# Kernel optimization log

Hardware: AMD Instinct MI355X
Metric: run time of the kernel (lower is better)

## Reference

```python
import jax, jax.numpy as jnp
import numpy as np

B, S, D, H, M = 2, 2048, 1024, 16, 4096
DH = D // H
EPS = 1e-6  # flax LayerNorm default
THETA = 10000.0


def layer_norm(x, scale, bias):
    m = jnp.mean(x, axis=-1, keepdims=True)
    v = jnp.var(x, axis=-1, keepdims=True)
    return (x - m) * jax.lax.rsqrt(v + EPS) * scale + bias


def apply_rope(xq, xk):
    # xq, xk: [B, S, H, DH]; rotate consecutive pairs as complex numbers
    half = DH // 2
    freqs = 1.0 / THETA ** (jnp.arange(0, DH, 2)[:half].astype(jnp.float32) / DH)
    t = jnp.arange(S, dtype=jnp.float32)
    ang = jnp.outer(t, freqs)                      # [S, half]
    cos = jnp.cos(ang)[None, :, None, :]           # [1, S, 1, half]
    sin = jnp.sin(ang)[None, :, None, :]

    def rot(x):
        xr = x.astype(jnp.float32).reshape(*x.shape[:-1], half, 2)
        a, b = xr[..., 0], xr[..., 1]
        out = jnp.stack((a * cos - b * sin, a * sin + b * cos), axis=-1)
        return out.reshape(*x.shape).astype(jnp.float32)

    return rot(xq), rot(xk)


def setup_inputs() -> dict:
    key = jax.random.key(0)
    ks = jax.random.split(key, 12)
    sd = 1.0 / np.sqrt(D)
    return {
        "x": jax.random.normal(ks[0], (B, S, D), jnp.float32),
        "ln1_s": jnp.ones((D,), jnp.float32),
        "ln1_b": jnp.zeros((D,), jnp.float32),
        "wk": jax.random.normal(ks[1], (D, D), jnp.float32) * sd,
        "wq": jax.random.normal(ks[2], (D, D), jnp.float32) * sd,
        "wv": jax.random.normal(ks[3], (D, D), jnp.float32) * sd,
        "wo": jax.random.normal(ks[4], (D, D), jnp.float32) * sd,
        "ln2_s": jnp.ones((D,), jnp.float32),
        "ln2_b": jnp.zeros((D,), jnp.float32),
        "w1": jax.random.normal(ks[5], (D, M), jnp.float32) * sd,
        "b1": jnp.zeros((M,), jnp.float32),
        "w2": jax.random.normal(ks[6], (M, D), jnp.float32) * (1.0 / np.sqrt(M)),
        "b2": jnp.zeros((D,), jnp.float32),
    }


def reference(x, ln1_s, ln1_b, wk, wq, wv, wo, ln2_s, ln2_b, w1, b1, w2, b2):
    h = layer_norm(x, ln1_s, ln1_b)
    xk = (h @ wk).reshape(B, S, H, DH)
    xq = (h @ wq).reshape(B, S, H, DH)
    xv = (h @ wv).reshape(B, S, H, DH)
    xq, xk = apply_rope(xq, xk)
    # scores: [B, H, S, S]
    scores = jnp.einsum("bqhd,bkhd->bhqk", xq, xk) / jnp.sqrt(jnp.float32(DH))
    attn = jax.nn.softmax(scores, axis=-1)
    ctx = jnp.einsum("bhqk,bkhd->bqhd", attn, xv).reshape(B, S, D)
    attn_out = ctx @ wo
    mlp_in = attn_out + x
    h2 = layer_norm(mlp_in, ln2_s, ln2_b)
    h2 = jax.nn.gelu(h2 @ w1 + b1)  # approximate gelu (jax default, matches source)
    h2 = h2 @ w2 + b2
    return h2 + mlp_in
```

## Files before the change

kernel.cpp:

```cpp
#include <hip/hip_runtime.h>
#include <stdint.h>

#define B_ 2
#define S_ 2048
#define D_ 1024
#define H_ 16
#define DH_ 64
#define M_ 4096
#define BS_ 4096

typedef __attribute__((ext_vector_type(8))) short short8;
typedef __attribute__((ext_vector_type(4))) float f32x4;

static __device__ __forceinline__ unsigned short f2bf(float f) {
  unsigned u = __float_as_uint(f);
  u += 0x7fffu + ((u >> 16) & 1u);
  return (unsigned short)(u >> 16);
}
static __device__ __forceinline__ float bf2f(unsigned short s) {
  return __uint_as_float(((unsigned)s) << 16);
}
static __device__ __forceinline__ f32x4 MFMA16(short8 a, short8 b, f32x4 c) {
  return __builtin_amdgcn_mfma_f32_16x16x32_bf16(a, b, c, 0, 0, 0);
}
static __device__ __forceinline__ void gload_lds16(const void* g, void* l) {
  __builtin_amdgcn_global_load_lds(
      (const __attribute__((address_space(1))) unsigned int*)g,
      (__attribute__((address_space(3))) unsigned int*)l, 16, 0, 0);
}
static __device__ __forceinline__ unsigned cvtpk_bf16(float lo, float hi) {
  unsigned r;
  asm("v_cvt_pk_bf16_f32 %0, %1, %2" : "=v"(r) : "v"(lo), "v"(hi));
  return r;
}
static __device__ __forceinline__ float gelu_f(float x) {
  float u = 0.7978845608028654f * (x + 0.044715f * x * x * x);
  return 0.5f * x * (1.0f + tanhf(u));
}

__global__ __launch_bounds__(256) void tcast_kernel(const float* __restrict__ in,
                                                    unsigned short* __restrict__ out,
                                                    int R, int C) {
  __shared__ float tile[32][33];
  int tx = threadIdx.x & 31, ty = threadIdx.x >> 5;
  int r0 = blockIdx.y * 32, c0 = blockIdx.x * 32;
#pragma unroll
  for (int i = 0; i < 4; ++i)
    tile[ty + i * 8][tx] = in[(size_t)(r0 + ty + i * 8) * C + c0 + tx];
  __syncthreads();
#pragma unroll
  for (int i = 0; i < 4; ++i)
    out[(size_t)(c0 + ty + i * 8) * R + r0 + tx] = f2bf(tile[tx][ty + i * 8]);
}

__global__ __launch_bounds__(256) void ln_kernel(const float* __restrict__ x,
                                                 const float* __restrict__ sc,
                                                 const float* __restrict__ bi,
                                                 unsigned short* __restrict__ out) {
  int row = blockIdx.x;
  int t = threadIdx.x;
  float4 v = ((const float4*)(x + (size_t)row * D_))[t];
  float s1 = v.x + v.y + v.z + v.w;
  float s2 = v.x * v.x + v.y * v.y + v.z * v.z + v.w * v.w;
#pragma unroll
  for (int m = 1; m < 64; m <<= 1) {
    s1 += __shfl_xor(s1, m);
    s2 += __shfl_xor(s2, m);
  }
  __shared__ float red[8];
  int w = t >> 6, l = t & 63;
  if (l == 0) { red[w] = s1; red[4 + w] = s2; }
  __syncthreads();
  s1 = red[0] + red[1] + red[2] + red[3];
  s2 = red[4] + red[5] + red[6] + red[7];
  float mean = s1 * (1.0f / D_);
  float var = s2 * (1.0f / D_) - mean * mean;
  float rstd = rsqrtf(var + 1e-6f);
  float4 scv = ((const float4*)sc)[t];
  float4 biv = ((const float4*)bi)[t];
  ushort4 o;
  o.x = f2bf((v.x - mean) * rstd * scv.x + biv.x);
  o.y = f2bf((v.y - mean) * rstd * scv.y + biv.y);
  o.z = f2bf((v.z - mean) * rstd * scv.z + biv.z);
  o.w = f2bf((v.w - mean) * rstd * scv.w + biv.w);
  ((ushort4*)out)[(size_t)row * (D_ / 4) + t] = o;
}

__global__ __launch_bounds__(256) void rope_kernel(unsigned short* __restrict__ t_,
                                                   float qscale) {
  size_t idx = (size_t)blockIdx.x * 256 + threadIdx.x;
  int c = (int)(idx & 7);
  size_t rowi = idx >> 3;
  int s = (int)(rowi & (S_ - 1));
  unsigned short* p = t_ + rowi * DH_ + c * 8;
  short8 v = *(const short8*)p;
  unsigned short o[8];
#pragma unroll
  for (int i = 0; i < 4; ++i) {
    int pi = c * 4 + i;
    float freq = exp2f(-(float)pi * 0.4152410118609203f);
    float ang = (float)s * freq;
    float sn, cs;
    sincosf(ang, &sn, &cs);
    float a = bf2f((unsigned short)v[2 * i]);
    float b = bf2f((unsigned short)v[2 * i + 1]);
    o[2 * i] = f2bf((a * cs - b * sn) * qscale);
    o[2 * i + 1] = f2bf((a * sn + b * cs) * qscale);
  }
  short8 ov;
#pragma unroll
  for (int i = 0; i < 8; ++i) ov[i] = (short)o[i];
  *(short8*)p = ov;
}

__global__ __launch_bounds__(256) void attn_kernel(const unsigned short* __restrict__ q,
                                                   const unsigned short* __restrict__ k,
                                                   const unsigned short* __restrict__ vt,
                                                   unsigned short* __restrict__ ctx) {
  __shared__ char smem[40960];
  const int tid = threadIdx.x, w = tid >> 6, l = tid & 63;
  const int g = l >> 4, qi = l & 15;
  char* Ps = smem + 32768 + w * 2048;
  int flat = blockIdx.y * 32 + blockIdx.x;
  int swz = (flat & 7) * 128 + (flat >> 3);
  const int bh = swz >> 5;
  const int b = bh >> 4, h = bh & 15;
  const int q0 = (swz & 31) * 64 + w * 16;

  const unsigned short* qbase = q + ((size_t)bh * S_ + q0 + qi) * DH_ + g * 8;
  short8 qf0 = *(const short8*)qbase;
  short8 qf1 = *(const short8*)(qbase + 32);

  const unsigned short* kb = k + (size_t)bh * S_ * DH_;
  const unsigned short* vb = vt + (size_t)bh * DH_ * S_;

  short8 onesB;
#pragma unroll
  for (int i = 0; i < 8; ++i) onesB[i] = (short)0x3F80;

  f32x4 o[4], l_acc;
#pragma unroll
  for (int dt = 0; dt < 4; ++dt) { f32x4 z = {0.f, 0.f, 0.f, 0.f}; o[dt] = z; }
  { f32x4 z = {0.f, 0.f, 0.f, 0.f}; l_acc = z; }

#define STAGE_KV(buf, kt)                                                        \
  {                                                                              \
    char* Ks_ = smem + (buf) * 16384;                                            \
    char* Vs_ = Ks_ + 8192;                                                      \
    _Pragma("unroll") for (int i = 0; i < 2; ++i) {                              \
      int slot = i * 256 + tid;                                                  \
      int r = slot >> 3, pc = slot & 7;                                          \
      int sc_ = pc ^ (r & 7);                                                    \
      gload_lds16(kb + (size_t)((kt) + r) * DH_ + sc_ * 8,                       \
                  Ks_ + (i * 4096 + w * 1024));                                  \
      gload_lds16(vb + (size_t)r * S_ + (kt) + sc_ * 8,                          \
                  Vs_ + (i * 4096 + w * 1024));                                  \
    }                                                                            \
  }

  STAGE_KV(0, 0);
  asm volatile("s_waitcnt vmcnt(0)" ::: "memory");
  __builtin_amdgcn_s_barrier();

  for (int t = 0; t < S_ / 64; ++t) {
    int buf = t & 1;
    if (t + 1 < S_ / 64) STAGE_KV(buf ^ 1, (t + 1) * 64);
    char* Ks = smem + buf * 16384;
    char* Vs = Ks + 8192;

#pragma unroll
    for (int jt = 0; jt < 4; ++jt) {
      int r = jt * 16 + qi;
      const char* krow = Ks + r * 128;
      short8 kf0 = *(const short8*)(krow + ((g ^ (r & 7)) << 4));
      short8 kf1 = *(const short8*)(krow + (((g + 4) ^ (r & 7)) << 4));
      f32x4 z = {0.f, 0.f, 0.f, 0.f};
      z = MFMA16(kf0, qf0, z);
      z = MFMA16(kf1, qf1, z);
      uint2 pk2;
      pk2.x = cvtpk_bf16(exp2f(z[0]), exp2f(z[1]));
      pk2.y = cvtpk_bf16(exp2f(z[2]), exp2f(z[3]));
      int slot = 2 * jt + (g >> 1);
      *(uint2*)(Ps + qi * 128 + ((slot ^ (qi & 7)) << 4) + (g & 1) * 8) = pk2;
    }

    short8 pa0 = *(const short8*)(Ps + qi * 128 + ((g ^ (qi & 7)) << 4));
    short8 pa1 = *(const short8*)(Ps + qi * 128 + (((g + 4) ^ (qi & 7)) << 4));
    l_acc = MFMA16(pa0, onesB, l_acc);
    l_acc = MFMA16(pa1, onesB, l_acc);
#pragma unroll
    for (int dt = 0; dt < 4; ++dt) {
      int r = dt * 16 + qi;
      const char* vrow = Vs + r * 128;
      short8 vf0 = *(const short8*)(vrow + ((g ^ (r & 7)) << 4));
      short8 vf1 = *(const short8*)(vrow + (((g + 4) ^ (r & 7)) << 4));
      o[dt] = MFMA16(pa0, vf0, o[dt]);
      o[dt] = MFMA16(pa1, vf1, o[dt]);
    }
    asm volatile("s_waitcnt vmcnt(0)" ::: "memory");
    __builtin_amdgcn_s_barrier();
  }

  float rl[4];
#pragma unroll
  for (int r = 0; r < 4; ++r) rl[r] = 1.0f / l_acc[r];
#pragma unroll
  for (int dt = 0; dt < 4; ++dt) {
#pragma unroll
    for (int r = 0; r < 4; ++r) {
      int s = q0 + 4 * g + r;
      ctx[((size_t)(b * S_) + s) * D_ + h * DH_ + dt * 16 + qi] =
          f2bf(o[dt][r] * rl[r]);
    }
  }
#undef STAGE_KV
}

template <int EPI>
__global__ __launch_bounds__(256) void gemm_bt(const unsigned short* __restrict__ A,
                                               const unsigned short* __restrict__ Bt,
                                               int K,
                                               const float* __restrict__ aux0,
                                               const float* __restrict__ aux1,
                                               void* __restrict__ out0,
                                               void* __restrict__ out1,
                                               void* __restrict__ out2) {
  __shared__ char smem[65536];
  int tid = threadIdx.x, w = tid >> 6, l = tid & 63;
  int wr = w >> 1, wc = w & 1;
  int gx = gridDim.x;
  int nwg = gx * gridDim.y;
  int flat = blockIdx.y * gx + blockIdx.x;
  int swz = (flat & 7) * (nwg >> 3) + (flat >> 3);
  int row0 = (swz / gx) * 128, col0 = (swz % gx) * 128;
  f32x4 acc[4][4];
#pragma unroll
  for (int mt = 0; mt < 4; ++mt)
#pragma unroll
    for (int nt = 0; nt < 4; ++nt) {
      f32x4 z = {0.f, 0.f, 0.f, 0.f};
      acc[mt][nt] = z;
    }
  int lr = l >> 3, lc = l & 7;

#define STAGE_AB(buf, kt)                                                        \
  {                                                                              \
    char* As_ = smem + (buf) * 32768;                                            \
    char* Bs_ = As_ + 16384;                                                     \
    _Pragma("unroll") for (int i = 0; i < 4; ++i) {                              \
      int rb = w * 32 + i * 8;                                                   \
      int r = rb + lr;                                                           \
      int sc_ = lc ^ (r & 7);                                                    \
      gload_lds16(A + (size_t)(row0 + r) * K + (kt) + sc_ * 8, As_ + rb * 128);  \
      gload_lds16(Bt + (size_t)(col0 + r) * K + (kt) + sc_ * 8, Bs_ + rb * 128); \
    }                                                                            \
  }

  STAGE_AB(0, 0);
  asm volatile("s_waitcnt vmcnt(0)" ::: "memory");
  __builtin_amdgcn_s_barrier();

  const int NT = K >> 6;
  for (int t = 0; t < NT; ++t) {
    int buf = t & 1;
    if (t + 1 < NT) STAGE_AB(buf ^ 1, (t + 1) * 64);
    char* As = smem + buf * 32768;
    char* Bs = As + 16384;
#pragma unroll
    for (int kf = 0; kf < 2; ++kf) {
      short8 af[4], bfr[4];
#pragma unroll
      for (int mt = 0; mt < 4; ++mt) {
        int r = wr * 64 + mt * 16 + (l & 15);
        int c = (l >> 4) + 4 * kf;
        af[mt] = *(const short8*)(As + r * 128 + ((c ^ (r & 7)) << 4));
      }
#pragma unroll
      for (int nt = 0; nt < 4; ++nt) {
        int r = wc * 64 + nt * 16 + (l & 15);
        int c = (l >> 4) + 4 * kf;
        bfr[nt] = *(const short8*)(Bs + r * 128 + ((c ^ (r & 7)) << 4));
      }
#pragma unroll
      for (int mt = 0; mt < 4; ++mt)
#pragma unroll
        for (int nt = 0; nt < 4; ++nt)
          acc[mt][nt] = MFMA16(af[mt], bfr[nt], acc[mt][nt]);
    }
    asm volatile("s_waitcnt vmcnt(0)" ::: "memory");
    __builtin_amdgcn_s_barrier();
  }
#undef STAGE_AB

#pragma unroll
  for (int mt = 0; mt < 4; ++mt) {
#pragma unroll
    for (int nt = 0; nt < 4; ++nt) {
      int grow0 = row0 + wr * 64 + mt * 16 + ((l >> 4) << 2);
      int gcol = col0 + wc * 64 + nt * 16 + (l & 15);
      if (EPI == 0) {
        int which = gcol >> 10;
        int d = gcol & 1023;
        int hh = d >> 6, dh = d & 63;
#pragma unroll
        for (int r = 0; r < 4; ++r) {
          int grow = grow0 + r;
          int b = grow >> 11, s = grow & 2047;
          float v = acc[mt][nt][r];
          if (which == 0)
            ((unsigned short*)out0)[(((size_t)(b * H_ + hh)) * S_ + s) * DH_ + dh] = f2bf(v);
          else if (which == 1)
            ((unsigned short*)out1)[(((size_t)(b * H_ + hh)) * S_ + s) * DH_ + dh] = f2bf(v);
          else
            ((unsigned short*)out2)[(((size_t)(b * H_ + hh)) * DH_ + dh) * S_ + s] = f2bf(v);
        }
      } else if (EPI == 1) {
        float* mo = (float*)out0;
#pragma unroll
        for (int r = 0; r < 4; ++r) {
          int grow = grow0 + r;
          mo[(size_t)grow * D_ + gcol] = acc[mt][nt][r] + aux0[(size_t)grow * D_ + gcol];
        }
      } else if (EPI == 2) {
        unsigned short* gq = (unsigned short*)out0;
        float bb = aux0[gcol];
#pragma unroll
        for (int r = 0; r < 4; ++r) {
          int grow = grow0 + r;
          gq[(size_t)grow * M_ + gcol] = f2bf(gelu_f(acc[mt][nt][r] + bb));
        }
      } else {
        float* po = (float*)out0;
        float bb = aux0[gcol];
#pragma unroll
        for (int r = 0; r < 4; ++r) {
          int grow = grow0 + r;
          po[(size_t)grow * D_ + gcol] =
              acc[mt][nt][r] + bb + aux1[(size_t)grow * D_ + gcol];
        }
      }
    }
  }
}

extern "C" void kernel_launch(void* const* d_in, const int* in_sizes, int n_in,
                              void* d_out, int out_size, void* d_ws, size_t ws_size,
                              hipStream_t stream) {
  const float* x = (const float*)d_in[0];
  const float* ln1s = (const float*)d_in[1];
  const float* ln1b = (const float*)d_in[2];
  const float* wk = (const float*)d_in[3];
  const float* wq = (const float*)d_in[4];
  const float* wv = (const float*)d_in[5];
  const float* wo = (const float*)d_in[6];
  const float* ln2s = (const float*)d_in[7];
  const float* ln2b = (const float*)d_in[8];
  const float* w1 = (const float*)d_in[9];
  const float* b1 = (const float*)d_in[10];
  const float* w2 = (const float*)d_in[11];
  const float* b2 = (const float*)d_in[12];

  char* ws = (char*)d_ws;
  unsigned short* wqkv_t = (unsigned short*)(ws);
  unsigned short* wo_t = (unsigned short*)(ws + 6291456);
  unsigned short* w1_t = (unsigned short*)(ws + 8388608);
  unsigned short* w2_t = (unsigned short*)(ws + 16777216);
  unsigned short* h_bf = (unsigned short*)(ws + 25165824);
  unsigned short* q_bf = (unsigned short*)(ws + 33554432);
  unsigned short* k_bf = (unsigned short*)(ws + 41943040);
  unsigned short* vt_bf = (unsigned short*)(ws + 50331648);
  unsigned short* ctx_bf = (unsigned short*)(ws + 58720256);
  float* mlp_in = (float*)(ws + 67108864);
  unsigned short* g_bf = (unsigned short*)(ws + 83886080);

  dim3 blk(256);
  tcast_kernel<<<dim3(32, 32), blk, 0, stream>>>(wq, wqkv_t, 1024, 1024);
  tcast_kernel<<<dim3(32, 32), blk, 0, stream>>>(wk, wqkv_t + 1048576, 1024, 1024);
  tcast_kernel<<<dim3(32, 32), blk, 0, stream>>>(wv, wqkv_t + 2097152, 1024, 1024);
  tcast_kernel<<<dim3(32, 32), blk, 0, stream>>>(wo, wo_t, 1024, 1024);
  tcast_kernel<<<dim3(128, 32), blk, 0, stream>>>(w1, w1_t, 1024, 4096);
  tcast_kernel<<<dim3(32, 128), blk, 0, stream>>>(w2, w2_t, 4096, 1024);
  ln_kernel<<<dim3(BS_), blk, 0, stream>>>(x, ln1s, ln1b, h_bf);
  gemm_bt<0><<<dim3(24, 32), blk, 0, stream>>>(h_bf, wqkv_t, 1024, nullptr, nullptr,
                                               q_bf, k_bf, vt_bf);
  rope_kernel<<<dim3(2048), blk, 0, stream>>>(q_bf, 0.125f * 1.4426950408889634f);
  rope_kernel<<<dim3(2048), blk, 0, stream>>>(k_bf, 1.0f);
  attn_kernel<<<dim3(32, 32), blk, 0, stream>>>(q_bf, k_bf, vt_bf, ctx_bf);
  gemm_bt<1><<<dim3(8, 32), blk, 0, stream>>>(ctx_bf, wo_t, 1024, x, nullptr,
                                              mlp_in, nullptr, nullptr);
  ln_kernel<<<dim3(BS_), blk, 0, stream>>>(mlp_in, ln2s, ln2b, h_bf);
  gemm_bt<2><<<dim3(32, 32), blk, 0, stream>>>(h_bf, w1_t, 1024, b1, nullptr,
                                               g_bf, nullptr, nullptr);
  gemm_bt<3><<<dim3(8, 32), blk, 0, stream>>>(g_bf, w2_t, 4096, b2, mlp_in,
                                              (float*)d_out, nullptr, nullptr);
}
```

Measured before the change: 381.1 us.

## Switch attention kernel to 32x32x16 MFMA with 128-query tiles per block

Rewrites the attention inner loop to use 32x32x16 bf16 MFMA instructions, with each wave handling 32 query rows instead of 16, so a block now covers 128 queries and the grid is halved. Each K/V tile staged in LDS is reused across twice as many queries, which cuts LDS fragment reads and global K/V traffic per query. It also raises wave priority around the MFMA sections. In exchange it uses more accumulator registers and larger per-wave P buffers, and launches half as many blocks, which may reduce occupancy.

```diff
diff --git a/kernel.cpp b/kernel.cpp
--- a/kernel.cpp
+++ b/kernel.cpp
@@ -11,6 +11,7 @@
 
 typedef __attribute__((ext_vector_type(8))) short short8;
 typedef __attribute__((ext_vector_type(4))) float f32x4;
+typedef __attribute__((ext_vector_type(16))) float f32x16;
 
 static __device__ __forceinline__ unsigned short f2bf(float f) {
   unsigned u = __float_as_uint(f);
@@ -22,6 +23,9 @@
 }
 static __device__ __forceinline__ f32x4 MFMA16(short8 a, short8 b, f32x4 c) {
   return __builtin_amdgcn_mfma_f32_16x16x32_bf16(a, b, c, 0, 0, 0);
+}
+static __device__ __forceinline__ f32x16 MFMA32(short8 a, short8 b, f32x16 c) {
+  return __builtin_amdgcn_mfma_f32_32x32x16_bf16(a, b, c, 0, 0, 0);
 }
 static __device__ __forceinline__ void gload_lds16(const void* g, void* l) {
   __builtin_amdgcn_global_load_lds(
@@ -117,19 +121,20 @@
                                                    const unsigned short* __restrict__ k,
                                                    const unsigned short* __restrict__ vt,
                                                    unsigned short* __restrict__ ctx) {
-  __shared__ char smem[40960];
+  __shared__ char smem[49152];
   const int tid = threadIdx.x, w = tid >> 6, l = tid & 63;
-  const int g = l >> 4, qi = l & 15;
-  char* Ps = smem + 32768 + w * 2048;
-  int flat = blockIdx.y * 32 + blockIdx.x;
-  int swz = (flat & 7) * 128 + (flat >> 3);
-  const int bh = swz >> 5;
+  const int lo = l & 31, hi = l >> 5;
+  char* Ps = smem + 32768 + w * 4096;
+  int flat = blockIdx.y * 16 + blockIdx.x;
+  int swz = (flat & 7) * 64 + (flat >> 3);
+  const int bh = swz >> 4;
   const int b = bh >> 4, h = bh & 15;
-  const int q0 = (swz & 31) * 64 + w * 16;
-
-  const unsigned short* qbase = q + ((size_t)bh * S_ + q0 + qi) * DH_ + g * 8;
-  short8 qf0 = *(const short8*)qbase;
-  short8 qf1 = *(const short8*)(qbase + 32);
+  const int q0 = (swz & 15) * 128 + w * 32;
+
+  const unsigned short* qbase = q + ((size_t)bh * S_ + q0 + lo) * DH_ + hi * 8;
+  short8 qf[4];
+#pragma unroll
+  for (int c = 0; c < 4; ++c) qf[c] = *(const short8*)(qbase + c * 16);
 
   const unsigned short* kb = k + (size_t)bh * S_ * DH_;
   const unsigned short* vb = vt + (size_t)bh * DH_ * S_;
@@ -138,10 +143,9 @@
 #pragma unroll
   for (int i = 0; i < 8; ++i) onesB[i] = (short)0x3F80;
 
-  f32x4 o[4], l_acc;
-#pragma unroll
-  for (int dt = 0; dt < 4; ++dt) { f32x4 z = {0.f, 0.f, 0.f, 0.f}; o[dt] = z; }
-  { f32x4 z = {0.f, 0.f, 0.f, 0.f}; l_acc = z; }
+  f32x16 o0, o1, lac;
+#pragma unroll
+  for (int i = 0; i < 16; ++i) { o0[i] = 0.f; o1[i] = 0.f; lac[i] = 0.f; }
 
 #define STAGE_KV(buf, kt)                                                        \
   {                                                                              \
@@ -169,49 +173,55 @@
     char* Vs = Ks + 8192;
 
 #pragma unroll
-    for (int jt = 0; jt < 4; ++jt) {
-      int r = jt * 16 + qi;
-      const char* krow = Ks + r * 128;
-      short8 kf0 = *(const short8*)(krow + ((g ^ (r & 7)) << 4));
-      short8 kf1 = *(const short8*)(krow + (((g + 4) ^ (r & 7)) << 4));
-      f32x4 z = {0.f, 0.f, 0.f, 0.f};
-      z = MFMA16(kf0, qf0, z);
-      z = MFMA16(kf1, qf1, z);
-      uint2 pk2;
-      pk2.x = cvtpk_bf16(exp2f(z[0]), exp2f(z[1]));
-      pk2.y = cvtpk_bf16(exp2f(z[2]), exp2f(z[3]));
-      int slot = 2 * jt + (g >> 1);
-      *(uint2*)(Ps + qi * 128 + ((slot ^ (qi & 7)) << 4) + (g & 1) * 8) = pk2;
+    for (int kt2 = 0; kt2 < 2; ++kt2) {
+      f32x16 z;
+#pragma unroll
+      for (int i = 0; i < 16; ++i) z[i] = 0.f;
+      __builtin_amdgcn_s_setprio(1);
+#pragma unroll
+      for (int c = 0; c < 4; ++c) {
+        int r = kt2 * 32 + lo;
+        short8 kf = *(const short8*)(Ks + r * 128 + (((hi + 2 * c) ^ (r & 7)) << 4));
+        z = MFMA32(kf, qf[c], z);
+      }
+      __builtin_amdgcn_s_setprio(0);
+      unsigned pk[8];
+#pragma unroll
+      for (int e = 0; e < 8; ++e)
+        pk[e] = cvtpk_bf16(exp2f(z[2 * e]), exp2f(z[2 * e + 1]));
+#pragma unroll
+      for (int s2 = 0; s2 < 4; ++s2) {
+        uint2 dd;
+        dd.x = pk[2 * s2];
+        dd.y = pk[2 * s2 + 1];
+        int slot = kt2 * 4 + s2;
+        *(uint2*)(Ps + lo * 128 + ((slot ^ (lo & 7)) << 4) + hi * 8) = dd;
+      }
     }
 
-    short8 pa0 = *(const short8*)(Ps + qi * 128 + ((g ^ (qi & 7)) << 4));
-    short8 pa1 = *(const short8*)(Ps + qi * 128 + (((g + 4) ^ (qi & 7)) << 4));
-    l_acc = MFMA16(pa0, onesB, l_acc);
-    l_acc = MFMA16(pa1, onesB, l_acc);
-#pragma unroll
-    for (int dt = 0; dt < 4; ++dt) {
-      int r = dt * 16 + qi;
-      const char* vrow = Vs + r * 128;
-      short8 vf0 = *(const short8*)(vrow + ((g ^ (r & 7)) << 4));
-      short8 vf1 = *(const short8*)(vrow + (((g + 4) ^ (r & 7)) << 4));
-      o[dt] = MFMA16(pa0, vf0, o[dt]);
-      o[dt] = MFMA16(pa1, vf1, o[dt]);
+    __builtin_amdgcn_s_setprio(1);
+#pragma unroll
+    for (int c = 0; c < 4; ++c) {
+      short8 pa = *(const short8*)(Ps + lo * 128 + (((2 * c + hi) ^ (lo & 7)) << 4));
+      lac = MFMA32(pa, onesB, lac);
+      int r0v = lo, r1v = 32 + lo;
+      short8 vf0 = *(const short8*)(Vs + r0v * 128 + (((2 * c + hi) ^ (r0v & 7)) << 4));
+      short8 vf1 = *(const short8*)(Vs + r1v * 128 + (((2 * c + hi) ^ (r1v & 7)) << 4));
+      o0 = MFMA32(pa, vf0, o0);
+      o1 = MFMA32(pa, vf1, o1);
     }
+    __builtin_amdgcn_s_setprio(0);
     asm volatile("s_waitcnt vmcnt(0)" ::: "memory");
     __builtin_amdgcn_s_barrier();
   }
 
-  float rl[4];
-#pragma unroll
-  for (int r = 0; r < 4; ++r) rl[r] = 1.0f / l_acc[r];
-#pragma unroll
-  for (int dt = 0; dt < 4; ++dt) {
-#pragma unroll
-    for (int r = 0; r < 4; ++r) {
-      int s = q0 + 4 * g + r;
-      ctx[((size_t)(b * S_) + s) * D_ + h * DH_ + dt * 16 + qi] =
-          f2bf(o[dt][r] * rl[r]);
-    }
+#pragma unroll
+  for (int r = 0; r < 16; ++r) {
+    float rl = 1.0f / lac[r];
+    int srow = q0 + (r & 3) + 8 * (r >> 2) + 4 * hi;
+    unsigned short* cp = ctx + ((size_t)(b * S_) + srow) * D_ + h * DH_ + lo;
+    cp[0] = f2bf(o0[r] * rl);
+    cp[32] = f2bf(o1[r] * rl);
   }
 #undef STAGE_KV
 }
@@ -385,7 +395,7 @@
                                                q_bf, k_bf, vt_bf);
   rope_kernel<<<dim3(2048), blk, 0, stream>>>(q_bf, 0.125f * 1.4426950408889634f);
   rope_kernel<<<dim3(2048), blk, 0, stream>>>(k_bf, 1.0f);
-  attn_kernel<<<dim3(32, 32), blk, 0, stream>>>(q_bf, k_bf, vt_bf, ctx_bf);
+  attn_kernel<<<dim3(16, 32), blk, 0, stream>>>(q_bf, k_bf, vt_bf, ctx_bf);
   gemm_bt<1><<<dim3(8, 32), blk, 0, stream>>>(ctx_bf, wo_t, 1024, x, nullptr,
                                               mlp_in, nullptr, nullptr);
   ln_kernel<<<dim3(BS_), blk, 0, stream>>>(mlp_in, ln2s, ln2b, h_bf);
```

Result: faster. 372.6 us (-2.2%).
